# Optimization experiments

Measured on AMD Instinct MI355X. Metric: run time of the kernel, lower is better.

The kernel has to match this reference:

```python
import jax, jax.numpy as jnp
import numpy as np

B, N, D = 32, 4096, 512
H, DH, NS = 8, 64, 16
DI = H * DH
HID = 2048
ITERS = 3
EPS = 1e-8
TAU = 1.0
SCALE = D ** -0.5


def _ln(x, w, b):
    mu = jnp.mean(x, axis=-1, keepdims=True)
    var = jnp.mean(jnp.square(x - mu), axis=-1, keepdims=True)
    return (x - mu) * jax.lax.rsqrt(var + 1e-5) * w + b


def _gumbel_hard(logits, g, tau, axis):
    # straight-through hard gumbel softmax (matches torch F.gumbel_softmax(hard=True))
    y = jax.nn.softmax((logits + g) / tau, axis=axis)
    hard = jax.nn.one_hot(jnp.argmax(y, axis=axis), y.shape[axis], axis=axis, dtype=y.dtype)
    return hard + y - jax.lax.stop_gradient(y)


def setup_inputs():
    key = jax.random.key(0)
    ks = jax.random.split(key, 16)
    w = lambda k, sh: (0.02 * jax.random.normal(k, sh)).astype(jnp.float32)
    gumbel = lambda k, sh: -jnp.log(-jnp.log(jax.random.uniform(k, sh, jnp.float32, 1e-6, 1.0 - 1e-6)))
    return {
        "inputs": jax.random.normal(ks[0], (B, N, D), jnp.float32),
        "slots_mu": jax.random.normal(ks[1], (1, 1, D), jnp.float32),
        "slots_logsigma": (0.05 * jax.random.normal(ks[2], (1, 1, D))).astype(jnp.float32),
        "ln_in_w": jnp.ones((D,), jnp.float32), "ln_in_b": jnp.zeros((D,), jnp.float32),
        "ln_s_w": jnp.ones((D,), jnp.float32), "ln_s_b": jnp.zeros((D,), jnp.float32),
        "ln_ff_w": jnp.ones((D,), jnp.float32), "ln_ff_b": jnp.zeros((D,), jnp.float32),
        "Wq": w(ks[3], (D, DI)), "bq": jnp.zeros((DI,), jnp.float32),
        "Wk": w(ks[4], (D, DI)), "bk": jnp.zeros((DI,), jnp.float32),
        "Wv": w(ks[5], (D, DI)), "bv": jnp.zeros((DI,), jnp.float32),
        "Wc": w(ks[6], (DI, D)), "bc": jnp.zeros((D,), jnp.float32),
        "Wih": w(ks[7], (3 * D, D)), "bih": jnp.zeros((3 * D,), jnp.float32),
        "Whh": w(ks[8], (3 * D, D)), "bhh": jnp.zeros((3 * D,), jnp.float32),
        "W1": w(ks[9], (D, HID)), "b1": jnp.zeros((HID,), jnp.float32),
        "W2": w(ks[10], (HID, D)), "b2": jnp.zeros((D,), jnp.float32),
        "Wkeep": w(ks[11], (D, 2)),
        "slot_noise": jax.random.normal(ks[12], (B, NS, D), jnp.float32),
        "g_keep": gumbel(ks[13], (B, NS, 2)),
        "g_route": gumbel(ks[14], (B, NS, N)),
    }


def reference(inputs, slots_mu, slots_logsigma, ln_in_w, ln_in_b, ln_s_w, ln_s_b,
              ln_ff_w, ln_ff_b, Wq, bq, Wk, bk, Wv, bv, Wc, bc, Wih, bih, Whh, bhh,
              W1, b1, W2, b2, Wkeep, slot_noise, g_keep, g_route):
    b = inputs.shape[0]
    x = _ln(inputs, ln_in_w, ln_in_b)                              # [b,n,d]
    k = (x @ Wk + bk).reshape(b, N, H, DH)                         # [b,n,h,dh]
    v = (x @ Wv + bv).reshape(b, N, H, DH)
    slots = slots_mu + jnp.exp(slots_logsigma) * slot_noise        # [b,ns,d]
    for _ in range(ITERS):
        slots_prev = slots
        s = _ln(slots, ln_s_w, ln_s_b)
        q = (s @ Wq + bq).reshape(b, NS, H, DH)                    # [b,ns,h,dh]
        dots = jnp.einsum('bihd,bjhd->bhij', q, k) * SCALE         # [b,h,ns,n]
        attn = jax.nn.softmax(dots, axis=-2)                       # softmax over slots
        attn = attn + EPS
        attn = attn / jnp.sum(attn, axis=-1, keepdims=True)        # L1-normalize over tokens
        upd = jnp.einsum('bjhd,bhij->bihd', v, attn).reshape(b, NS, DI)
        upd = upd @ Wc + bc                                        # [b,ns,d]
        # PyTorch GRUCell
        gi = upd @ Wih.T + bih
        gh = slots_prev @ Whh.T + bhh
        gi_r, gi_z, gi_n = jnp.split(gi, 3, axis=-1)
        gh_r, gh_z, gh_n = jnp.split(gh, 3, axis=-1)
        r = jax.nn.sigmoid(gi_r + gh_r)
        z = jax.nn.sigmoid(gi_z + gh_z)
        nn_ = jnp.tanh(gi_n + r * gh_n)
        slots = (1.0 - z) * nn_ + z * slots_prev
        h = jax.nn.relu(_ln(slots, ln_ff_w, ln_ff_b) @ W1 + b1)
        slots = slots + h @ W2 + b2
    keep = _gumbel_hard(slots @ Wkeep, g_keep, TAU, axis=-1)[..., -1]  # [b,ns]
    slots = slots * keep[..., None]
    dots2 = jnp.einsum('bid,bjd->bij', slots, x) * SCALE           # [b,ns,n]
    attn2 = _gumbel_hard(dots2, g_route, 1.0, axis=-2)             # hard route over slots
    attn2 = jnp.transpose(attn2, (0, 2, 1))                        # [b,n,ns]
    corr_token = jnp.einsum('bjd,bij->bid', slots, attn2)          # [b,n,d]
    return corr_token
```

## Files before the change

### kernel.cpp

```cpp
#include <hip/hip_runtime.h>
#include <hip/hip_bf16.h>
#include <math.h>

constexpr int Bn = 32, Nn = 4096, Dn = 512, NSn = 16, HIn = 128;
constexpr float kScale = 0.04419417382415922f;
constexpr float kEps = 1e-8f;

typedef __attribute__((ext_vector_type(8))) short short8;
typedef __attribute__((ext_vector_type(4))) float f32x4;

__device__ __forceinline__ float wred(float v) {
#pragma unroll
  for (int m = 32; m > 0; m >>= 1) v += __shfl_xor(v, m);
  return v;
}
__device__ __forceinline__ double wredd(double v) {
#pragma unroll
  for (int m = 32; m > 0; m >>= 1) v += __shfl_xor(v, m);
  return v;
}

__device__ __forceinline__ unsigned short f2bf(float x) {
  unsigned u = __float_as_uint(x);
  unsigned r = (u + 0x7fffu + ((u >> 16) & 1u)) >> 16;
  return (unsigned short)r;
}
__device__ __forceinline__ float bf2f(unsigned short h) {
  return __uint_as_float(((unsigned)h) << 16);
}
__device__ __forceinline__ unsigned packhm(float x) {
  unsigned short h = f2bf(x);
  unsigned short m = f2bf(x - bf2f(h));
  return (unsigned)h | ((unsigned)m << 16);
}
__device__ __forceinline__ unsigned pack2x(float x0, float x1, unsigned& mo) {
  unsigned p0 = packhm(x0), p1 = packhm(x1);
  mo = (p0 >> 16) | (p1 & 0xffff0000u);
  return (p0 & 0xffffu) | (p1 << 16);
}

__global__ __launch_bounds__(256) void k_tsplit(const float* __restrict__ in, unsigned short* __restrict__ inT,
                                                float* __restrict__ psum, float* __restrict__ psqs) {
  __shared__ float tile[64][65];
  int b = blockIdx.z, j0 = blockIdx.x * 64, d0 = blockIdx.y * 64;
  int t = threadIdx.x;
  int rr = t >> 4, c4 = (t & 15) * 4;
  float4 v4[4];
#pragma unroll
  for (int e = 0; e < 4; ++e) {
    int r = e * 16 + rr;
    v4[e] = *reinterpret_cast<const float4*>(&in[((size_t)b * Nn + j0 + r) * Dn + d0 + c4]);
    tile[r][c4] = v4[e].x; tile[r][c4 + 1] = v4[e].y;
    tile[r][c4 + 2] = v4[e].z; tile[r][c4 + 3] = v4[e].w;
  }
  __syncthreads();
  float rs_s, rs_q;
  {
    int r = t >> 2, q = t & 3;
    float s = 0.0f, qq = 0.0f;
#pragma unroll
    for (int c = 0; c < 16; ++c) {
      float x = tile[r][q * 16 + c];
      s += x; qq += x * x;
    }
    s += __shfl_xor(s, 1); s += __shfl_xor(s, 2);
    qq += __shfl_xor(qq, 1); qq += __shfl_xor(qq, 2);
    rs_s = s; rs_q = qq;
  }
  unsigned short pv[16];
#pragma unroll
  for (int e = 0; e < 4; ++e) {
    pv[e * 4 + 0] = f2bf(v4[e].x);
    pv[e * 4 + 1] = f2bf(v4[e].y);
    pv[e * 4 + 2] = f2bf(v4[e].z);
    pv[e * 4 + 3] = f2bf(v4[e].w);
  }
  __syncthreads();
  unsigned short (*u16t)[130] = reinterpret_cast<unsigned short(*)[130]>(tile);
#pragma unroll
  for (int e = 0; e < 4; ++e) {
    int r = e * 16 + rr;
    u16t[r][c4] = pv[e * 4 + 0]; u16t[r][c4 + 1] = pv[e * 4 + 1];
    u16t[r][c4 + 2] = pv[e * 4 + 2]; u16t[r][c4 + 3] = pv[e * 4 + 3];
  }
  {
    int r = t >> 2, q = t & 3;
    if (q == 0) {
      size_t pi = ((size_t)b * Nn + j0 + r) * 8 + blockIdx.y;
      psum[pi] = rs_s;
      psqs[pi] = rs_q;
    }
  }
  __syncthreads();
#pragma unroll
  for (int e = 0; e < 4; ++e) {
    int dloc = e * 16 + rr;
    unsigned short o0 = u16t[c4][dloc], o1 = u16t[c4 + 1][dloc];
    unsigned short o2 = u16t[c4 + 2][dloc], o3 = u16t[c4 + 3][dloc];
    uint2 o;
    o.x = (unsigned)o0 | ((unsigned)o1 << 16);
    o.y = (unsigned)o2 | ((unsigned)o3 << 16);
    *reinterpret_cast<uint2*>(&inT[((size_t)b * Dn + d0 + dloc) * Nn + j0 + c4]) = o;
  }
}

__global__ __launch_bounds__(256) void k_initln(const float* __restrict__ smu, const float* __restrict__ sls,
                                                const float* __restrict__ noise,
                                                const float* __restrict__ lnsw, const float* __restrict__ lnsb,
                                                float* __restrict__ slots, float* __restrict__ sln,
                                                const float* __restrict__ psum, const float* __restrict__ psqs,
                                                float* __restrict__ mu, float* __restrict__ rsig) {
  int t = threadIdx.x;
  if (blockIdx.x >= Bn * NSn) {
    int row = (blockIdx.x - Bn * NSn) * 256 + t;
    float s = 0.0f, q = 0.0f;
#pragma unroll
    for (int e = 0; e < 8; ++e) {
      s += psum[(size_t)row * 8 + e];
      q += psqs[(size_t)row * 8 + e];
    }
    float m = s * (1.0f / 512.0f);
    float var = q * (1.0f / 512.0f) - m * m;
    mu[row] = m;
    rsig[row] = 1.0f / sqrtf(var + 1e-5f);
    return;
  }
  int r = blockIdx.x;
  __shared__ float red[8];
  float sn[2];
#pragma unroll
  for (int j = 0; j < 2; ++j) {
    int c = j * 256 + t;
    sn[j] = smu[c] + expf(sls[c]) * noise[(size_t)r * Dn + c];
  }
  float s = sn[0] + sn[1], q = sn[0] * sn[0] + sn[1] * sn[1];
  s = wred(s); q = wred(q);
  if ((t & 63) == 0) { red[t >> 6] = s; red[4 + (t >> 6)] = q; }
  __syncthreads();
  float S = red[0] + red[1] + red[2] + red[3];
  float Q = red[4] + red[5] + red[6] + red[7];
  float m = S * (1.0f / 512.0f);
  float rs = 1.0f / sqrtf(Q * (1.0f / 512.0f) - m * m + 1e-5f);
#pragma unroll
  for (int j = 0; j < 2; ++j) {
    int c = j * 256 + t;
    slots[(size_t)r * Dn + c] = sn[j];
    sln[(size_t)r * Dn + c] = (sn[j] - m) * rs * lnsw[c] + lnsb[c];
  }
}

template <bool TRANS, bool RELU, bool ADD>
__global__ __launch_bounds__(256) void k_gemm_sm(const float* __restrict__ A, const float* __restrict__ W,
                                                 const float* __restrict__ bias, float* __restrict__ out,
                                                 int Nc, int K) {
  __shared__ float as_[64][17];
  __shared__ float ws_[16][65];
  int m0 = blockIdx.y * 64, n0 = blockIdx.x * 64;
  int t = threadIdx.x, tx = t & 15, ty = t >> 4;
  float acc[4][4] = {};
  float pa[4], pw[4];
  auto loadA = [&](int k0) {
#pragma unroll
    for (int e = 0; e < 4; ++e) {
      int idx = t + e * 256;
      int r = idx >> 4, c = idx & 15;
      pa[e] = A[(size_t)(m0 + r) * K + k0 + c];
    }
  };
  auto loadW = [&](int k0) {
#pragma unroll
    for (int e = 0; e < 4; ++e) {
      int idx = t + e * 256;
      if (!TRANS) {
        int r = idx >> 6, c = idx & 63;
        pw[e] = W[(size_t)(k0 + r) * Nc + n0 + c];
      } else {
        int r = idx >> 4, c = idx & 15;
        pw[e] = W[(size_t)(n0 + r) * K + k0 + c];
      }
    }
  };
  loadA(0); loadW(0);
  for (int k0 = 0; k0 < K; k0 += 16) {
#pragma unroll
    for (int e = 0; e < 4; ++e) {
      int idx = t + e * 256;
      int r = idx >> 4, c = idx & 15;
      as_[r][c] = pa[e];
    }
#pragma unroll
    for (int e = 0; e < 4; ++e) {
      int idx = t + e * 256;
      if (!TRANS) {
        int r = idx >> 6, c = idx & 63;
        ws_[r][c] = pw[e];
      } else {
        int r = idx >> 4, c = idx & 15;
        ws_[c][r] = pw[e];
      }
    }
    __syncthreads();
    if (k0 + 16 < K) { loadA(k0 + 16); loadW(k0 + 16); }
#pragma unroll
    for (int kc = 0; kc < 16; ++kc) {
      float av[4], wv[4];
#pragma unroll
      for (int i = 0; i < 4; ++i) av[i] = as_[ty * 4 + i][kc];
#pragma unroll
      for (int j = 0; j < 4; ++j) wv[j] = ws_[kc][tx * 4 + j];
#pragma unroll
      for (int i = 0; i < 4; ++i)
#pragma unroll
        for (int j = 0; j < 4; ++j) acc[i][j] += av[i] * wv[j];
    }
    __syncthreads();
  }
#pragma unroll
  for (int i = 0; i < 4; ++i)
#pragma unroll
    for (int j = 0; j < 4; ++j) {
      int m = m0 + ty * 4 + i, n = n0 + tx * 4 + j;
      float v = acc[i][j] + (bias ? bias[n] : 0.0f);
      if (RELU) v = fmaxf(v, 0.0f);
      if (ADD) v += out[(size_t)m * Nc + n];
      out[(size_t)m * Nc + n] = v;
    }
}

// ... 315 lines not shown
  }
  float s = sn[0] + sn[1], q = sn[0] * sn[0] + sn[1] * sn[1];
  s = wred(s); q = wred(q);
  if ((t & 63) == 0) { red[t >> 6] = s; red[4 + (t >> 6)] = q; }
  __syncthreads();
  float S = red[0] + red[1] + red[2] + red[3];
  float Q = red[4] + red[5] + red[6] + red[7];
  float m = S * (1.0f / 512.0f);
  float rs = 1.0f / sqrtf(Q * (1.0f / 512.0f) - m * m + 1e-5f);
#pragma unroll
  for (int j = 0; j < 2; ++j) {
    int c = j * 256 + t;
    size_t idx = (size_t)r * 512 + c;
    slots[idx] = sn[j];
    sln[idx] = (sn[j] - m) * rs * lnsw[c] + lnsb[c];
  }
}

__global__ __launch_bounds__(256) void k_mh(const float* __restrict__ Wq, const float* __restrict__ Wk,
                                            float* __restrict__ Ms) {
  int h = blockIdx.z, k0 = blockIdx.y * 64, d0 = blockIdx.x * 64;
  __shared__ float qa[64][65];
  __shared__ float ka[64][65];
  int t = threadIdx.x, tx = t & 15, ty = t >> 4;
#pragma unroll
  for (int e = 0; e < 16; ++e) {
    int idx = t + e * 256;
    int r = idx >> 6, c = idx & 63;
    qa[c][r] = Wq[(size_t)(k0 + r) * Dn + h * 64 + c];
    ka[c][r] = Wk[(size_t)(d0 + r) * Dn + h * 64 + c];
  }
  __syncthreads();
  float acc[4][4] = {};
#pragma unroll 4
  for (int c = 0; c < 64; ++c) {
    float av[4], bv[4];
#pragma unroll
    for (int i = 0; i < 4; ++i) av[i] = qa[c][ty * 4 + i];
#pragma unroll
    for (int j = 0; j < 4; ++j) bv[j] = ka[c][tx * 4 + j];
#pragma unroll
    for (int i = 0; i < 4; ++i)
#pragma unroll
      for (int j = 0; j < 4; ++j) acc[i][j] += av[i] * bv[j];
  }
#pragma unroll
  for (int i = 0; i < 4; ++i)
#pragma unroll
    for (int j = 0; j < 4; ++j)
      Ms[(size_t)(k0 + ty * 4 + i) * 4096 + h * 512 + d0 + tx * 4 + j] = acc[i][j];
}

__global__ __launch_bounds__(256) void k_vbias_bcih(const float* __restrict__ Wk, const float* __restrict__ bq,
                                                    const float* __restrict__ lnw, float* __restrict__ vb_raw,
                                                    float* __restrict__ vb_s, const float* __restrict__ bc,
                                                    const float* __restrict__ Wih, const float* __restrict__ bih,
                                                    float* __restrict__ bcih) {
  __shared__ float cbuf[512];
  int t = threadIdx.x;
  if (blockIdx.x < 2) {
    cbuf[t] = bq[t]; cbuf[256 + t] = bq[256 + t];
    __syncthreads();
    int d = blockIdx.x * 256 + t;
    float vb[8] = {};
    const float4* wr = reinterpret_cast<const float4*>(Wk + (size_t)d * Dn);
#pragma unroll 8
    for (int c4 = 0; c4 < 128; ++c4) {
      float4 wv = wr[c4];
      int h = c4 >> 4;
      int c = c4 * 4;
      vb[h] += wv.x * cbuf[c] + wv.y * cbuf[c + 1] + wv.z * cbuf[c + 2] + wv.w * cbuf[c + 3];
    }
    float lw = lnw[d];
#pragma unroll
    for (int h = 0; h < 8; ++h) {
      vb_raw[h * 512 + d] = vb[h];
      vb_s[h * 512 + d] = kScale * lw * vb[h];
    }
  } else {
    cbuf[t] = bc[t]; cbuf[256 + t] = bc[256 + t];
    __syncthreads();
    int n = (blockIdx.x - 2) * 256 + t;
    const float4* wr = reinterpret_cast<const float4*>(Wih + (size_t)n * Dn);
    float a = 0.0f;
#pragma unroll 8
    for (int c4 = 0; c4 < 128; ++c4) {
      float4 wv = wr[c4];
      int c = c4 * 4;
      a += wv.x * cbuf[c] + wv.y * cbuf[c + 1] + wv.z * cbuf[c + 2] + wv.w * cbuf[c + 3];
    }
    bcih[n] = a + bih[n];
  }
}

__global__ __launch_bounds__(256) void k_mfold_consts(float* __restrict__ Ms, const float* __restrict__ Wq,
                                                      const float* __restrict__ bk, const float* __restrict__ lnw,
                                                      const float* __restrict__ lnb, float* __restrict__ avec,
                                                      float* __restrict__ bvec, const float* __restrict__ vb_raw,
                                                      const float* __restrict__ bq, float* __restrict__ aconst,
                                                      float* __restrict__ bconst) {
  int t = threadIdx.x;
  if (blockIdx.x < 16) {
    __shared__ float lws[512], lbs[512], bks[512];
    lws[t] = lnw[t]; lws[256 + t] = lnw[256 + t];
    lbs[t] = lnb[t]; lbs[256 + t] = lnb[256 + t];
    bks[t] = bk[t]; bks[256 + t] = bk[256 + t];
    __syncthreads();
    int g = blockIdx.x * 256 + t;
    int k = g >> 3, h = g & 7;
    float* mr = Ms + (size_t)k * 4096 + h * 512;
    float mlnb = 0.0f, mlnw = 0.0f;
    for (int d = 0; d < 512; d += 4) {
      float4 m4 = *reinterpret_cast<const float4*>(mr + d);
      mlnb += m4.x * lbs[d] + m4.y * lbs[d + 1] + m4.z * lbs[d + 2] + m4.w * lbs[d + 3];
      mlnw += m4.x * lws[d] + m4.y * lws[d + 1] + m4.z * lws[d + 2] + m4.w * lws[d + 3];
      float4 o4 = {m4.x * kScale * lws[d], m4.y * kScale * lws[d + 1],
                   m4.z * kScale * lws[d + 2], m4.w * kScale * lws[d + 3]};
      *reinterpret_cast<float4*>(mr + d) = o4;
    }
    float wqdot = 0.0f;
    const float* qr = Wq + (size_t)k * Dn + h * 64;
    for (int c = 0; c < 64; c += 4) {
      float4 q4 = *reinterpret_cast<const float4*>(qr + c);
      wqdot += q4.x * bks[h * 64 + c] + q4.y * bks[h * 64 + c + 1] +
               q4.z * bks[h * 64 + c + 2] + q4.w * bks[h * 64 + c + 3];
    }
    avec[h * 512 + k] = kScale * (mlnb + wqdot);
    bvec[h * 512 + k] = kScale * mlnw;
  } else {
    __shared__ float r1[256], r2[256], r3[256];
    for (int h = 0; h < 8; ++h) {
      float p1 = 0.0f, p2 = 0.0f, p3 = 0.0f;
      for (int d = t; d < 512; d += 256) {
        float vr = vb_raw[h * 512 + d];
        p1 += lnb[d] * vr;
        p2 += lnw[d] * vr;
      }
      if (t < 64) p3 = bq[h * 64 + t] * bk[h * 64 + t];
      r1[t] = p1; r2[t] = p2; r3[t] = p3;
      __syncthreads();
      for (int s = 128; s > 0; s >>= 1) {
        if (t < s) { r1[t] += r1[t + s]; r2[t] += r2[t + s]; r3[t] += r3[t + s]; }
        __syncthreads();
      }
      if (t == 0) {
        aconst[h] = kScale * (r1[0] + r3[0]);
        bconst[h] = kScale * r2[0];
      }
      __syncthreads();
    }
  }
}

__global__ __launch_bounds__(256) void k_dots(const unsigned short* __restrict__ inT, const unsigned short* __restrict__ qkt,
                                              const float* __restrict__ alpha, const float* __restrict__ beta,
                                              const float* __restrict__ mu, const float* __restrict__ rsig,
                                              unsigned short* __restrict__ A, float* __restrict__ Spart,
                                              float* __restrict__ c1part) {
  __shared__ __align__(16) unsigned short xs_h[128][40];
  __shared__ __align__(16) unsigned short us_h[128][40];
  __shared__ __align__(16) float redbuf[1536];

  int b = blockIdx.y, jt = blockIdx.x, j0 = jt * 128;
  int t = threadIdx.x, w = t >> 6, l = t & 63;
  int lc = l & 15, lg = l >> 4, koff = lg * 8;
  const size_t tbase = (size_t)b * Dn * Nn + j0;
  const size_t ubase = (size_t)b * HIn * Dn;

  f32x4 acc[2][8];
#pragma unroll
  for (int i = 0; i < 2; ++i)
#pragma unroll
    for (int j2 = 0; j2 < 8; ++j2) acc[i][j2] = {0.0f, 0.0f, 0.0f, 0.0f};

  int xdl = t >> 3;
  int xj4 = (t & 7) * 4;

  uint2 px[4];
  uint2 nu[4];
#pragma unroll
  for (int e = 0; e < 4; ++e)
    px[e] = *reinterpret_cast<const uint2*>(&inT[tbase + (size_t)xdl * Nn + e * 32 + xj4]);
#pragma unroll
  for (int e = 0; e < 4; ++e) {
    int idx = t + e * 256;
    int j = idx >> 3, dg = idx & 7;
    nu[e] = *reinterpret_cast<const uint2*>(&qkt[ubase + (size_t)j * Dn + dg * 4]);
  }

  for (int k0 = 0; k0 < 512; k0 += 32) {
#pragma unroll
    for (int e = 0; e < 4; ++e) {
      const unsigned short* pe = reinterpret_cast<const unsigned short*>(&px[e]);
#pragma unroll
      for (int i = 0; i < 4; ++i) {
        int j = e * 32 + xj4 + i;
        int ds = xdl ^ (((j >> 4) & 3) << 3);
        xs_h[j][ds] = pe[i];
      }
    }
#pragma unroll
    for (int e = 0; e < 4; ++e) {
      int idx = t + e * 256;
      int j = idx >> 3, dg = idx & 7;
      *reinterpret_cast<uint2*>(&us_h[j][dg * 4]) = nu[e];
    }
    if (k0 + 32 < 512) {
#pragma unroll
      for (int e = 0; e < 4; ++e)
        px[e] = *reinterpret_cast<const uint2*>(&inT[tbase + (size_t)(k0 + 32 + xdl) * Nn + e * 32 + xj4]);
#pragma unroll
      for (int e = 0; e < 4; ++e) {
        int idx = t + e * 256;
        int j = idx >> 3, dg = idx & 7;
        nu[e] = *reinterpret_cast<const uint2*>(&qkt[ubase + (size_t)j * Dn + k0 + 32 + dg * 4]);
      }
    }
    __syncthreads();
    int row0 = w * 32 + lc, row1 = row0 + 16;
    int sw0 = ((row0 >> 4) & 3) << 3, sw1 = ((row1 >> 4) & 3) << 3;
    short8 ah0 = *reinterpret_cast<const short8*>(&xs_h[row0][koff ^ sw0]);
    short8 ah1 = *reinterpret_cast<const short8*>(&xs_h[row1][koff ^ sw1]);
#pragma unroll
    for (int ht = 0; ht < 8; ++ht) {
      short8 bh = *reinterpret_cast<const short8*>(&us_h[ht * 16 + lc][koff]);
      acc[0][ht] = __builtin_amdgcn_mfma_f32_16x16x32_bf16(ah0, bh, acc[0][ht], 0, 0, 0);
      acc[1][ht] = __builtin_amdgcn_mfma_f32_16x16x32_bf16(ah1, bh, acc[1][ht], 0, 0, 0);
    }
    __syncthreads();
  }

  float* rsL = redbuf;
  float* muL = rsL + 128;
  float* aL = rsL + 256;
  float* bL = rsL + 384;
  float (*sredS)[128] = reinterpret_cast<float(*)[128]>(rsL + 512);
  float (*sredC)[128] = reinterpret_cast<float(*)[128]>(rsL + 512 + 4 * 128);
  if (t < 128) {
    rsL[t] = rsig[(size_t)b * Nn + j0 + t];
    muL[t] = mu[(size_t)b * Nn + j0 + t];
    aL[t] = alpha[b * HIn + t];
    bL[t] = beta[b * HIn + t];
  }
  __syncthreads();

  float sS[8] = {}, sC[8] = {};
#pragma unroll
  for (int jt2 = 0; jt2 < 2; ++jt2) {
    int jbase = w * 32 + jt2 * 16 + lg * 4;
#pragma unroll
    for (int ht = 0; ht < 8; ++ht) {
      int hi = ht * 16 + lc;
      float av = aL[hi], bv = bL[hi];
      float v[4], rs4[4], mr4[4];
#pragma unroll
      for (int r = 0; r < 4; ++r) {
        int jr = jbase + r;
        rs4[r] = rsL[jr];
        mr4[r] = muL[jr] * rs4[r];
        v[r] = acc[jt2][ht][r] * rs4[r] + av - mr4[r] * bv;
      }
      float mx[4] = {v[0], v[1], v[2], v[3]};
#pragma unroll
      for (int m = 1; m <= 8; m <<= 1)
#pragma unroll
        for (int r = 0; r < 4; ++r) mx[r] = fmaxf(mx[r], __shfl_xor(mx[r], m));
      float e4[4], ss[4];
#pragma unroll
      for (int r = 0; r < 4; ++r) { e4[r] = expf(v[r] - mx[r]); ss[r] = e4[r]; }
#pragma unroll
      for (int m = 1; m <= 8; m <<= 1)
#pragma unroll
        for (int r = 0; r < 4; ++r) ss[r] += __shfl_xor(ss[r], m);
      float ps = 0.0f, pc = 0.0f;
      float p0 = e4[0] / ss[0] + kEps, p1 = e4[1] / ss[1] + kEps;
      float p2 = e4[2] / ss[2] + kEps, p3 = e4[3] / ss[3] + kEps;
      unsigned h01 = (unsigned)f2bf(p0 * rs4[0]) | ((unsigned)f2bf(p1 * rs4[1]) << 16);
      unsigned h23 = (unsigned)f2bf(p2 * rs4[2]) | ((unsigned)f2bf(p3 * rs4[3]) << 16);
      uint2 o2 = {h01, h23};
      ps = p0 + p1 + p2 + p3;
      pc = p0 * mr4[0] + p1 * mr4[1] + p2 * mr4[2] + p3 * mr4[3];
      *reinterpret_cast<uint2*>(&A[(size_t)(b * HIn + hi) * Nn + j0 + jbase]) = o2;
      ps += __shfl_xor(ps, 16); ps += __shfl_xor(ps, 32);
      pc += __shfl_xor(pc, 16); pc += __shfl_xor(pc, 32);
      sS[ht] += ps; sC[ht] += pc;
    }
  }
  if (l < 16) {
#pragma unroll
    for (int ht = 0; ht < 8; ++ht) {
      sredS[w][ht * 16 + l] = sS[ht];
      sredC[w][ht * 16 + l] = sC[ht];
    }
  }
  __syncthreads();
  if (t < 128) {
    float s_ = sredS[0][t] + sredS[1][t] + sredS[2][t] + sredS[3][t];
    float c_ = sredC[0][t] + sredC[1][t] + sredC[2][t] + sredC[3][t];
    int sub = (b * 32 + jt) * HIn + t;
    Spart[sub] = s_;
    c1part[sub] = c_;
  }
}

__global__ __launch_bounds__(256) void k_ax(const unsigned short* __restrict__ Au, const unsigned short* __restrict__ inT,
                                            float* __restrict__ AXp) {
  __shared__ __align__(16) unsigned short as_h[128][40];
  __shared__ __align__(16) unsigned short xs_h[64][40];

  int lid = blockIdx.x + 8 * (blockIdx.y + 2 * blockIdx.z);
  int d0 = (lid >> 6) * 64;
  int rest = lid & 63;
  int kp = rest & 1, b = rest >> 1;

  int t = threadIdx.x, w = t >> 6, l = t & 63;
  int lc = l & 15, lg = l >> 4, koff = lg * 8;
  const size_t abase = (size_t)b * HIn * Nn + (size_t)kp * 2048;
  const size_t xbase = ((size_t)b * Dn + d0) * Nn + (size_t)kp * 2048;

  f32x4 acc[2][4];
#pragma unroll
  for (int i = 0; i < 2; ++i)
#pragma unroll
    for (int j2 = 0; j2 < 4; ++j2) acc[i][j2] = {0.0f, 0.0f, 0.0f, 0.0f};

  uint2 pa[4];
  uint2 px[2];
#pragma unroll
  for (int e = 0; e < 4; ++e) {
    int idx = t + e * 256;
    int hi = idx >> 3, sl = idx & 7;
    pa[e] = *reinterpret_cast<const uint2*>(&Au[abase + (size_t)hi * Nn + sl * 4]);
  }
#pragma unroll
  for (int e = 0; e < 2; ++e) {
    int idx = t + e * 256;
    int d = idx >> 3, jg = idx & 7;
    px[e] = *reinterpret_cast<const uint2*>(&inT[xbase + (size_t)d * Nn + jg * 4]);
  }

  for (int c0 = 0; c0 < 2048; c0 += 32) {
#pragma unroll
    for (int e = 0; e < 4; ++e) {
      int idx = t + e * 256;
      int hi = idx >> 3, sl = idx & 7;
      *reinterpret_cast<uint2*>(&as_h[hi][sl * 4]) = pa[e];
    }
#pragma unroll
    for (int e = 0; e < 2; ++e) {
      int idx = t + e * 256;
      int d = idx >> 3, jg = idx & 7;
      *reinterpret_cast<uint2*>(&xs_h[d][jg * 4]) = px[e];
    }
    if (c0 + 32 < 2048) {
#pragma unroll
      for (int e = 0; e < 4; ++e) {
        int idx = t + e * 256;
        int hi = idx >> 3, sl = idx & 7;
        pa[e] = *reinterpret_cast<const uint2*>(&Au[abase + (size_t)hi * Nn + c0 + 32 + sl * 4]);
      }
#pragma unroll
      for (int e = 0; e < 2; ++e) {
        int idx = t + e * 256;
        int d = idx >> 3, jg = idx & 7;
        px[e] = *reinterpret_cast<const uint2*>(&inT[xbase + (size_t)d * Nn + c0 + 32 + jg * 4]);
      }
    }
    __syncthreads();
    short8 ah0 = *reinterpret_cast<const short8*>(&as_h[w * 32 + lc][koff]);
    short8 ah1 = *reinterpret_cast<const short8*>(&as_h[w * 32 + 16 + lc][koff]);
#pragma unroll
    for (int dt = 0; dt < 4; ++dt) {
      short8 bh = *reinterpret_cast<const short8*>(&xs_h[dt * 16 + lc][koff]);
      acc[0][dt] = __builtin_amdgcn_mfma_f32_16x16x32_bf16(ah0, bh, acc[0][dt], 0, 0, 0);
      acc[1][dt] = __builtin_amdgcn_mfma_f32_16x16x32_bf16(ah1, bh, acc[1][dt], 0, 0, 0);
    }
    __syncthreads();
  }

  const size_t obase = (((size_t)kp * Bn + b) * HIn) * Dn + d0;
#pragma unroll
  for (int jt2 = 0; jt2 < 2; ++jt2) {
#pragma unroll
    for (int dt = 0; dt < 4; ++dt) {
#pragma unroll
      for (int r = 0; r < 4; ++r) {
        int hi = w * 32 + jt2 * 16 + lg * 4 + r;
        int d = dt * 16 + lc;
        AXp[obase + (size_t)hi * Dn + d] = acc[jt2][dt][r];
      }
    }
  }
}

__global__ __launch_bounds__(256) void k_updS(const float* __restrict__ AXp, const float* __restrict__ Spart,
                                              const float* __restrict__ c1part, const float* __restrict__ lnw,
                                              const float* __restrict__ lnb, const float* __restrict__ Wv,
                                              const float* __restrict__ bv, float* __restrict__ upd) {
  int b = blockIdx.y, hi = blockIdx.x, h = hi >> 4, i = hi & 15;
  __shared__ float vx[512];
  __shared__ float red[256];
  __shared__ float sSC[2];
  int t = threadIdx.x;
  if (t < 64) {
    float vs = 0.0f, vc = 0.0f;
    if (t < 32) {
      vs = Spart[(size_t)(b * 32 + t) * HIn + hi];
      vc = c1part[(size_t)(b * 32 + t) * HIn + hi];
    }
    vs = wred(vs); vc = wred(vc);
    if (t == 0) { sSC[0] = vs; sSC[1] = vc; }
  }
  __syncthreads();
  float c1v = sSC[1];
  float invS = 1.0f / sSC[0];
  for (int d = t; d < Dn; d += 256) {
    float G = AXp[((size_t)(0 * Bn + b) * HIn + hi) * Dn + d]
            + AXp[((size_t)(1 * Bn + b) * HIn + hi) * Dn + d];
    vx[d] = lnw[d] * (G - c1v) * invS + lnb[d];
  }
  __syncthreads();
  int cc = t & 63, qd = t >> 6;
  float p = 0.0f;
  for (int d = qd * 128; d < qd * 128 + 128; ++d) p += vx[d] * Wv[(size_t)d * Dn + h * 64 + cc];
  red[t] = p;
  __syncthreads();
  if (qd == 0) {
    float v = red[cc] + red[64 + cc] + red[128 + cc] + red[192 + cc] + bv[h * 64 + cc];
    upd[(size_t)(b * NSn + i) * Dn + h * 64 + cc] = v;
  }
}

__global__ __launch_bounds__(256) void k_gruln(const float* __restrict__ gi, const float* __restrict__ gh,
                                               float* __restrict__ slots, float* __restrict__ slnff,
                                               const float* __restrict__ lnffw, const float* __restrict__ lnffb) {
  int r = blockIdx.x, t = threadIdx.x;
  __shared__ float red[8];
  float sn[2];
#pragma unroll
  for (int j = 0; j < 2; ++j) {
    int c = j * 256 + t;
    float gir = gi[(size_t)r * 1536 + c];
    float giz = gi[(size_t)r * 1536 + 512 + c];
    float gin = gi[(size_t)r * 1536 + 1024 + c];
    float ghr = gh[(size_t)r * 1536 + c];
    float ghz = gh[(size_t)r * 1536 + 512 + c];
    float ghn = gh[(size_t)r * 1536 + 1024 + c];
    float rg = 1.0f / (1.0f + expf(-(gir + ghr)));
    float zg = 1.0f / (1.0f + expf(-(giz + ghz)));
    float ng = tanhf(gin + rg * ghn);
    sn[j] = (1.0f - zg) * ng + zg * slots[(size_t)r * Dn + c];
  }
  float s = sn[0] + sn[1], q = sn[0] * sn[0] + sn[1] * sn[1];
  s = wred(s); q = wred(q);
  if ((t & 63) == 0) { red[t >> 6] = s; red[4 + (t >> 6)] = q; }
  __syncthreads();
  float S = red[0] + red[1] + red[2] + red[3];
  float Q = red[4] + red[5] + red[6] + red[7];
  float m = S * (1.0f / 512.0f);
  float rs = 1.0f / sqrtf(Q * (1.0f / 512.0f) - m * m + 1e-5f);
#pragma unroll
  for (int j = 0; j < 2; ++j) {
    int c = j * 256 + t;
    slots[(size_t)r * Dn + c] = sn[j];
    slnff[(size_t)r * Dn + c] = (sn[j] - m) * rs * lnffw[c] + lnffb[c];
  }
}

__global__ __launch_bounds__(256) void k_route_out(const float* __restrict__ in, const float* __restrict__ slots,
                                                   const float* __restrict__ lnw, const float* __restrict__ lnb,
                                                   const float* __restrict__ Wkeep, const float* __restrict__ gk,
                                                   const float* __restrict__ mu, const float* __restrict__ rsig,
                                                   const float* __restrict__ g_route, float* __restrict__ out) {
  int b = blockIdx.y, j0 = blockIdx.x * 128;
  __shared__ __align__(16) float sl[16 * 516];
  __shared__ __align__(16) float lw[512];
  __shared__ __align__(16) float xs[16][132];
  __shared__ double lgd[128][17];
  __shared__ int besti[128];
  __shared__ double swdL[16], sbdL[16];
  int t = threadIdx.x, tx = t & 15, ty = t >> 4;
  int wv_ = t >> 6, lane = t & 63;

  for (int idx = t; idx < 2048; idx += 256) {
    int i = idx >> 7, c = idx & 127;
    *reinterpret_cast<float4*>(&sl[i * 516 + c * 4]) =
        *reinterpret_cast<const float4*>(&slots[(size_t)(b * NSn + i) * Dn + c * 4]);
  }
  if (t < 128)
    *reinterpret_cast<float4*>(&lw[t * 4]) = *reinterpret_cast<const float4*>(&lnw[t * 4]);
  __syncthreads();

#pragma unroll
  for (int qi = 0; qi < 4; ++qi) {
    int i = wv_ * 4 + qi;
    float* srow = &sl[i * 516];
    float sv[8];
#pragma unroll
    for (int e = 0; e < 8; ++e) sv[e] = srow[lane * 8 + e];
    double d0 = 0.0, d1 = 0.0;
#pragma unroll
    for (int e = 0; e < 8; ++e) {
      int d = lane * 8 + e;
      d0 += (double)sv[e] * (double)Wkeep[d * 2];
      d1 += (double)sv[e] * (double)Wkeep[d * 2 + 1];
    }
    d0 = wredd(d0);
    d1 = wredd(d1);
    int keepi = 0;
    if (lane == 0) keepi = ((d1 + (double)gk[(b * NSn + i) * 2 + 1]) > (d0 + (double)gk[(b * NSn + i) * 2])) ? 1 : 0;
    keepi = __shfl(keepi, 0);
    if (!keepi) {
#pragma unroll
      for (int e = 0; e < 8; ++e) { srow[lane * 8 + e] = 0.0f; sv[e] = 0.0f; }
    }
    double pw = 0.0, pb = 0.0;
#pragma unroll
    for (int e = 0; e < 8; ++e) {
      int d = lane * 8 + e;
      pw += (double)sv[e] * (double)lnw[d];
      pb += (double)sv[e] * (double)lnb[d];
    }
    pw = wredd(pw);
    pb = wredd(pb);
    if (lane == 0) { swdL[i] = pw; sbdL[i] = pb; }
  }

  float acc[8] = {};
  double accd[8] = {};
  const size_t inbase = ((size_t)b * Nn + j0) * Dn;

  float pre[8];
#pragma unroll
  for (int e = 0; e < 8; ++e) {
    int idx = t + e * 256;
    int r = idx >> 4, c = idx & 15;
    pre[e] = in[inbase + (size_t)r * Dn + c];
  }
  __syncthreads();

  for (int k0 = 0; k0 < Dn; k0 += 16) {
#pragma unroll
    for (int e = 0; e < 8; ++e) {
      int idx = t + e * 256;
      int r = idx >> 4, c = idx & 15;
      xs[c][r] = pre[e] * lw[k0 + c];
    }
    __syncthreads();
    float nxt[8] = {};
    if (k0 + 16 < Dn) {
#pragma unroll
      for (int e = 0; e < 8; ++e) {
        int idx = t + e * 256;
        int r = idx >> 4, c = idx & 15;
        nxt[e] = in[inbase + (size_t)r * Dn + k0 + 16 + c];
      }
    }
#pragma unroll
    for (int kc = 0; kc < 16; ++kc) {
      float sv = sl[tx * 516 + k0 + kc];
      float4 x0 = *reinterpret_cast<const float4*>(&xs[kc][ty * 8]);
      float4 x1 = *reinterpret_cast<const float4*>(&xs[kc][ty * 8 + 4]);
      acc[0] += x0.x * sv; acc[1] += x0.y * sv; acc[2] += x0.z * sv; acc[3] += x0.w * sv;
      acc[4] += x1.x * sv; acc[5] += x1.y * sv; acc[6] += x1.z * sv; acc[7] += x1.w * sv;
    }
    if ((k0 & 127) == 112) {
#pragma unroll
      for (int e = 0; e < 8; ++e) { accd[e] += (double)acc[e]; acc[e] = 0.0f; }
    }
#pragma unroll
    for (int e = 0; e < 8; ++e) pre[e] = nxt[e];
    __syncthreads();
  }

  double sw_i = swdL[tx], sb_i = sbdL[tx];
#pragma unroll
  for (int r = 0; r < 8; ++r) {
    int j = ty * 8 + r;
    double rsj = (double)rsig[(size_t)b * Nn + j0 + j];
    double muj = (double)mu[(size_t)b * Nn + j0 + j];
    double g = (double)g_route[((size_t)b * NSn + tx) * Nn + j0 + j];
    lgd[j][tx] = (double)kScale * (rsj * accd[r] + sb_i - muj * rsj * sw_i) + g;
  }
  __syncthreads();
  if (t < 128) {
    double best = lgd[t][0];
    int bi = 0;
#pragma unroll
    for (int i = 1; i < 16; ++i) {
      double v = lgd[t][i];
      if (v > best) { best = v; bi = i; }
    }
    besti[t] = bi;
  }
  __syncthreads();
  for (int idx = t; idx < 128 * 128; idx += 256) {
    int j = idx >> 7, c = idx & 127;
    *reinterpret_cast<float4*>(&out[inbase + (size_t)j * Dn + c * 4]) =
        *reinterpret_cast<const float4*>(&sl[besti[j] * 516 + c * 4]);
  }
}

extern "C" void kernel_launch(void* const* d_in, const int* in_sizes, int n_in,
                              void* d_out, int out_size, void* d_ws, size_t ws_size,
                              hipStream_t stream) {
  (void)in_sizes; (void)n_in; (void)out_size; (void)ws_size;
  const float* in = (const float*)d_in[0];
  const float* slots_mu = (const float*)d_in[1];
  const float* slots_ls = (const float*)d_in[2];
  const float* ln_in_w = (const float*)d_in[3];
  const float* ln_in_b = (const float*)d_in[4];
  const float* ln_s_w = (const float*)d_in[5];
  const float* ln_s_b = (const float*)d_in[6];
  const float* ln_ff_w = (const float*)d_in[7];
  const float* ln_ff_b = (const float*)d_in[8];
  const float* Wq = (const float*)d_in[9];
  const float* bq = (const float*)d_in[10];
  const float* Wk = (const float*)d_in[11];
  const float* bk = (const float*)d_in[12];
  const float* Wv = (const float*)d_in[13];
  const float* bv = (const float*)d_in[14];
  const float* Wc = (const float*)d_in[15];
  const float* bc = (const float*)d_in[16];
  const float* Wih = (const float*)d_in[17];
  const float* bih = (const float*)d_in[18];
  const float* Whh = (const float*)d_in[19];
  const float* bhh = (const float*)d_in[20];
  const float* W1 = (const float*)d_in[21];
  const float* b1 = (const float*)d_in[22];
  const float* W2 = (const float*)d_in[23];
  const float* b2 = (const float*)d_in[24];
  const float* Wkeep = (const float*)d_in[25];
  const float* noise = (const float*)d_in[26];
  const float* g_keep = (const float*)d_in[27];
  const float* g_route = (const float*)d_in[28];
  float* out = (float*)d_out;
  unsigned short* inTu = (unsigned short*)d_out;

  char* wptr = (char*)d_ws;
  auto alloc = [&](size_t bytes) {
    char* p = wptr;
    wptr += (bytes + 255) & ~(size_t)255;
    return p;
  };
  float* mu = (float*)alloc((size_t)Bn * Nn * 4);
  float* rsig = (float*)alloc((size_t)Bn * Nn * 4);
  float* psum = (float*)alloc((size_t)Bn * Nn * 8 * 4);
  float* psqs = (float*)alloc((size_t)Bn * Nn * 8 * 4);
  float* slots = (float*)alloc((size_t)Bn * NSn * Dn * 4);
  float* sln = (float*)alloc((size_t)Bn * NSn * Dn * 4);
  unsigned short* qkt = (unsigned short*)alloc((size_t)Bn * HIn * Dn * 2);
  float* alpha = (float*)alloc((size_t)Bn * HIn * 4);
  float* beta = (float*)alloc((size_t)Bn * HIn * 4);
  unsigned short* Abuf = (unsigned short*)alloc((size_t)Bn * HIn * Nn * 2);
  float* Spart = (float*)alloc((size_t)Bn * 32 * HIn * 4);
  float* c1part = (float*)alloc((size_t)Bn * 32 * HIn * 4);
  float* AXp = (float*)alloc((size_t)2 * Bn * HIn * Dn * 4);
  float* updb = (float*)alloc((size_t)Bn * NSn * Dn * 4);
  float* gibuf = (float*)alloc((size_t)Bn * NSn * 1536 * 4);
  float* ghbuf = (float*)alloc((size_t)Bn * NSn * 1536 * 4);
  float* hbuf = (float*)alloc((size_t)Bn * NSn * 2048 * 4);
  float* ffp = (float*)alloc((size_t)4 * 512 * 512 * 4);
  float* T1 = (float*)alloc((size_t)Dn * 1536 * 4);
  float* WhhT = (float*)alloc((size_t)Dn * 1536 * 4);
  float* bcih = (float*)alloc((size_t)1536 * 4);
  float* Ms = (float*)alloc((size_t)Dn * 4096 * 4);
  float* vb_raw = (float*)alloc((size_t)4096 * 4);
  float* vb_s = (float*)alloc((size_t)4096 * 4);
  float* avec = (float*)alloc((size_t)4096 * 4);
  float* bvec = (float*)alloc((size_t)4096 * 4);
  float* aconst = (float*)alloc((size_t)8 * 4);
  float* bconst = (float*)alloc((size_t)8 * 4);

  k_tsplit<<<dim3(Nn / 64, Dn / 64, Bn), 256, 0, stream>>>(in, inTu, psum, psqs);
  k_gemm_sm<true, false, false><<<dim3(24, 8), 256, 0, stream>>>(Wc, Wih, nullptr, T1, 1536, 512);
  k_transp<<<dim3(512 / 64, 1536 / 64), 256, 0, stream>>>(Whh, WhhT, 1536, 512);
  k_vbias_bcih<<<8, 256, 0, stream>>>(Wk, bq, ln_in_w, vb_raw, vb_s, bc, Wih, bih, bcih);
  k_mh<<<dim3(8, 8, 8), 256, 0, stream>>>(Wq, Wk, Ms);
  k_mfold_consts<<<17, 256, 0, stream>>>(Ms, Wq, bk, ln_in_w, ln_in_b, avec, bvec,
                                         vb_raw, bq, aconst, bconst);
  k_initln<<<Bn * NSn + Bn * Nn / 256, 256, 0, stream>>>(slots_mu, slots_ls, noise, ln_s_w, ln_s_b,
                                                         slots, sln, psum, psqs, mu, rsig);

  for (int it = 0; it < 3; ++it) {
    k_qum_ab<<<dim3(96, 8), 256, 0, stream>>>(sln, Ms, vb_s, qkt, avec, bvec, aconst, bconst, alpha, beta);
    k_dots<<<dim3(Nn / 128, Bn), 256, 0, stream>>>(inTu, qkt, alpha, beta, mu, rsig, Abuf, Spart, c1part);
    k_ax<<<dim3(Dn / 64, 2, Bn), 256, 0, stream>>>(Abuf, inTu, AXp);
    k_updS<<<dim3(HIn, Bn), 256, 0, stream>>>(AXp, Spart, c1part, ln_in_w, ln_in_b, Wv, bv, updb);
    k_ggm<<<dim3(24, 8, 2), 256, 0, stream>>>(updb, T1, bcih, slots, WhhT, bhh, gibuf, ghbuf);
    k_gruln<<<Bn * NSn, 256, 0, stream>>>(gibuf, ghbuf, slots, sln, ln_ff_w, ln_ff_b);
    k_mm<true, false><<<dim3(32, 8, 1), 256, 0, stream>>>(sln, 512, W1, 2048, b1, hbuf, 2048, 512);
    k_mm<false, true><<<dim3(8, 8, 4), 256, 0, stream>>>(hbuf, 2048, W2, 512, nullptr, ffp, 512, 512);
    k_w2ln<<<Bn * NSn, 256, 0, stream>>>(ffp, b2, slots, sln, ln_s_w, ln_s_b);
  }

  k_route_out<<<dim3(Nn / 128, Bn), 256, 0, stream>>>(in, slots, ln_in_w, ln_in_b, Wkeep, g_keep,
                                                      mu, rsig, g_route, out);
}
```

Baseline: 1.071 ms.

## Load MFMA operands directly from global memory, dropping LDS staging in dots and ax

k_tsplit now also writes a row-major bf16 copy of the inputs, so k_dots can read each A-fragment as a contiguous 16-byte global load instead of staging the transposed copy through shared memory. k_ax similarly reads its A and X fragments straight from global memory. Both kernels lose their LDS tiles and per-step barriers. The cost is an extra 128MB bf16 write in the preprocessing kernel, plus global loads that are less coalesced and rely on L2/L1 to serve the operands that several waves share.

```diff
diff --git a/kernel.cpp b/kernel.cpp
--- a/kernel.cpp
+++ b/kernel.cpp
@@ -40,6 +40,7 @@
 }
 
 __global__ __launch_bounds__(256) void k_tsplit(const float* __restrict__ in, unsigned short* __restrict__ inT,
+                                                unsigned short* __restrict__ Xp,
                                                 float* __restrict__ psum, float* __restrict__ psqs) {
   __shared__ float tile[64][65];
   int b = blockIdx.z, j0 = blockIdx.x * 64, d0 = blockIdx.y * 64;
@@ -74,6 +75,14 @@
     pv[e * 4 + 1] = f2bf(v4[e].y);
     pv[e * 4 + 2] = f2bf(v4[e].z);
     pv[e * 4 + 3] = f2bf(v4[e].w);
+  }
+#pragma unroll
+  for (int e = 0; e < 4; ++e) {
+    int r = e * 16 + rr;
+    uint2 o;
+    o.x = (unsigned)pv[e * 4 + 0] | ((unsigned)pv[e * 4 + 1] << 16);
+    o.y = (unsigned)pv[e * 4 + 2] | ((unsigned)pv[e * 4 + 3] << 16);
+    *reinterpret_cast<uint2*>(&Xp[((size_t)b * Nn + j0 + r) * Dn + d0 + c4]) = o;
   }
   __syncthreads();
   unsigned short (*u16t)[130] = reinterpret_cast<unsigned short(*)[130]>(tile);
@@ -695,19 +704,16 @@
   }
 }
 
-__global__ __launch_bounds__(256) void k_dots(const unsigned short* __restrict__ inT, const unsigned short* __restrict__ qkt,
+__global__ __launch_bounds__(256) void k_dots(const unsigned short* __restrict__ Xp, const unsigned short* __restrict__ qkt,
                                               const float* __restrict__ alpha, const float* __restrict__ beta,
                                               const float* __restrict__ mu, const float* __restrict__ rsig,
                                               unsigned short* __restrict__ A, float* __restrict__ Spart,
                                               float* __restrict__ c1part) {
-  __shared__ __align__(16) unsigned short xs_h[128][40];
-  __shared__ __align__(16) unsigned short us_h[128][40];
   __shared__ __align__(16) float redbuf[1536];
 
   int b = blockIdx.y, jt = blockIdx.x, j0 = jt * 128;
   int t = threadIdx.x, w = t >> 6, l = t & 63;
   int lc = l & 15, lg = l >> 4, koff = lg * 8;
-  const size_t tbase = (size_t)b * Dn * Nn + j0;
   const size_t ubase = (size_t)b * HIn * Dn;
 
   f32x4 acc[2][8];
@@ -716,61 +722,21 @@
 #pragma unroll
     for (int j2 = 0; j2 < 8; ++j2) acc[i][j2] = {0.0f, 0.0f, 0.0f, 0.0f};
 
-  int xdl = t >> 3;
-  int xj4 = (t & 7) * 4;
-
-  uint2 px[4];
-  uint2 nu[4];
-#pragma unroll
-  for (int e = 0; e < 4; ++e)
-    px[e] = *reinterpret_cast<const uint2*>(&inT[tbase + (size_t)xdl * Nn + e * 32 + xj4]);
-#pragma unroll
-  for (int e = 0; e < 4; ++e) {
-    int idx = t + e * 256;
-    int j = idx >> 3, dg = idx & 7;
-    nu[e] = *reinterpret_cast<const uint2*>(&qkt[ubase + (size_t)j * Dn + dg * 4]);
-  }
-
+  int row0 = w * 32 + lc, row1 = row0 + 16;
+  const unsigned short* xr0 = &Xp[((size_t)b * Nn + j0 + row0) * Dn + koff];
+  const unsigned short* xr1 = &Xp[((size_t)b * Nn + j0 + row1) * Dn + koff];
+  const unsigned short* ur = &qkt[ubase + (size_t)lc * Dn + koff];
+
+#pragma unroll 4
   for (int k0 = 0; k0 < 512; k0 += 32) {
-#pragma unroll
-    for (int e = 0; e < 4; ++e) {
-      const unsigned short* pe = reinterpret_cast<const unsigned short*>(&px[e]);
-#pragma unroll
-      for (int i = 0; i < 4; ++i) {
-        int j = e * 32 + xj4 + i;
-        int ds = xdl ^ (((j >> 4) & 3) << 3);
-        xs_h[j][ds] = pe[i];
-      }
-    }
-#pragma unroll
-    for (int e = 0; e < 4; ++e) {
-      int idx = t + e * 256;
-      int j = idx >> 3, dg = idx & 7;
-      *reinterpret_cast<uint2*>(&us_h[j][dg * 4]) = nu[e];
-    }
-    if (k0 + 32 < 512) {
-#pragma unroll
-      for (int e = 0; e < 4; ++e)
-        px[e] = *reinterpret_cast<const uint2*>(&inT[tbase + (size_t)(k0 + 32 + xdl) * Nn + e * 32 + xj4]);
-#pragma unroll
-      for (int e = 0; e < 4; ++e) {
-        int idx = t + e * 256;
-        int j = idx >> 3, dg = idx & 7;
-        nu[e] = *reinterpret_cast<const uint2*>(&qkt[ubase + (size_t)j * Dn + k0 + 32 + dg * 4]);
-      }
-    }
-    __syncthreads();
-    int row0 = w * 32 + lc, row1 = row0 + 16;
-    int sw0 = ((row0 >> 4) & 3) << 3, sw1 = ((row1 >> 4) & 3) << 3;
-    short8 ah0 = *reinterpret_cast<const short8*>(&xs_h[row0][koff ^ sw0]);
-    short8 ah1 = *reinterpret_cast<const short8*>(&xs_h[row1][koff ^ sw1]);
+    short8 a0 = *reinterpret_cast<const short8*>(&xr0[k0]);
+    short8 a1 = *reinterpret_cast<const short8*>(&xr1[k0]);
 #pragma unroll
     for (int ht = 0; ht < 8; ++ht) {
-      short8 bh = *reinterpret_cast<const short8*>(&us_h[ht * 16 + lc][koff]);
-      acc[0][ht] = __builtin_amdgcn_mfma_f32_16x16x32_bf16(ah0, bh, acc[0][ht], 0, 0, 0);
-      acc[1][ht] = __builtin_amdgcn_mfma_f32_16x16x32_bf16(ah1, bh, acc[1][ht], 0, 0, 0);
-    }
-    __syncthreads();
+      short8 bh = *reinterpret_cast<const short8*>(&ur[(size_t)(ht * 16) * Dn + k0]);
+      acc[0][ht] = __builtin_amdgcn_mfma_f32_16x16x32_bf16(a0, bh, acc[0][ht], 0, 0, 0);
+      acc[1][ht] = __builtin_amdgcn_mfma_f32_16x16x32_bf16(a1, bh, acc[1][ht], 0, 0, 0);
+    }
   }
 
   float* rsL = redbuf;
@@ -848,9 +814,6 @@
 
 __global__ __launch_bounds__(256) void k_ax(const unsigned short* __restrict__ Au, const unsigned short* __restrict__ inT,
                                             float* __restrict__ AXp) {
-  __shared__ __align__(16) unsigned short as_h[128][40];
-  __shared__ __align__(16) unsigned short xs_h[64][40];
-
   int lid = blockIdx.x + 8 * (blockIdx.y + 2 * blockIdx.z);
   int d0 = (lid >> 6) * 64;
   int rest = lid & 63;
@@ -858,8 +821,6 @@
 
   int t = threadIdx.x, w = t >> 6, l = t & 63;
   int lc = l & 15, lg = l >> 4, koff = lg * 8;
-  const size_t abase = (size_t)b * HIn * Nn + (size_t)kp * 2048;
-  const size_t xbase = ((size_t)b * Dn + d0) * Nn + (size_t)kp * 2048;
 
   f32x4 acc[2][4];
 #pragma unroll
@@ -867,58 +828,21 @@
 #pragma unroll
     for (int j2 = 0; j2 < 4; ++j2) acc[i][j2] = {0.0f, 0.0f, 0.0f, 0.0f};
 
-  uint2 pa[4];
-  uint2 px[2];
-#pragma unroll
-  for (int e = 0; e < 4; ++e) {
-    int idx = t + e * 256;
-    int hi = idx >> 3, sl = idx & 7;
-    pa[e] = *reinterpret_cast<const uint2*>(&Au[abase + (size_t)hi * Nn + sl * 4]);
-  }
-#pragma unroll
-  for (int e = 0; e < 2; ++e) {
-    int idx = t + e * 256;
-    int d = idx >> 3, jg = idx & 7;
-    px[e] = *reinterpret_cast<const uint2*>(&inT[xbase + (size_t)d * Nn + jg * 4]);
-  }
-
+  int hi0 = w * 32 + lc, hi1 = hi0 + 16;
+  const unsigned short* ar0 = &Au[(size_t)b * HIn * Nn + (size_t)hi0 * Nn + (size_t)kp * 2048 + koff];
+  const unsigned short* ar1 = &Au[(size_t)b * HIn * Nn + (size_t)hi1 * Nn + (size_t)kp * 2048 + koff];
+  const unsigned short* xr = &inT[((size_t)b * Dn + d0 + lc) * Nn + (size_t)kp * 2048 + koff];
+
+#pragma unroll 4
   for (int c0 = 0; c0 < 2048; c0 += 32) {
-#pragma unroll
-    for (int e = 0; e < 4; ++e) {
-      int idx = t + e * 256;
-      int hi = idx >> 3, sl = idx & 7;
-      *reinterpret_cast<uint2*>(&as_h[hi][sl * 4]) = pa[e];
-    }
-#pragma unroll
-    for (int e = 0; e < 2; ++e) {
-      int idx = t + e * 256;
-      int d = idx >> 3, jg = idx & 7;
-      *reinterpret_cast<uint2*>(&xs_h[d][jg * 4]) = px[e];
-    }
-    if (c0 + 32 < 2048) {
-#pragma unroll
-      for (int e = 0; e < 4; ++e) {
-        int idx = t + e * 256;
-        int hi = idx >> 3, sl = idx & 7;
-        pa[e] = *reinterpret_cast<const uint2*>(&Au[abase + (size_t)hi * Nn + c0 + 32 + sl * 4]);
-      }
-#pragma unroll
-      for (int e = 0; e < 2; ++e) {
-        int idx = t + e * 256;
-        int d = idx >> 3, jg = idx & 7;
-        px[e] = *reinterpret_cast<const uint2*>(&inT[xbase + (size_t)d * Nn + c0 + 32 + jg * 4]);
-      }
-    }
-    __syncthreads();
-    short8 ah0 = *reinterpret_cast<const short8*>(&as_h[w * 32 + lc][koff]);
-    short8 ah1 = *reinterpret_cast<const short8*>(&as_h[w * 32 + 16 + lc][koff]);
+    short8 a0 = *reinterpret_cast<const short8*>(&ar0[c0]);
+    short8 a1 = *reinterpret_cast<const short8*>(&ar1[c0]);
 #pragma unroll
     for (int dt = 0; dt < 4; ++dt) {
-      short8 bh = *reinterpret_cast<const short8*>(&xs_h[dt * 16 + lc][koff]);
-      acc[0][dt] = __builtin_amdgcn_mfma_f32_16x16x32_bf16(ah0, bh, acc[0][dt], 0, 0, 0);
-      acc[1][dt] = __builtin_amdgcn_mfma_f32_16x16x32_bf16(ah1, bh, acc[1][dt], 0, 0, 0);
-    }
-    __syncthreads();
+      short8 bh = *reinterpret_cast<const short8*>(&xr[(size_t)(dt * 16) * Nn + c0]);
+      acc[0][dt] = __builtin_amdgcn_mfma_f32_16x16x32_bf16(a0, bh, acc[0][dt], 0, 0, 0);
+      acc[1][dt] = __builtin_amdgcn_mfma_f32_16x16x32_bf16(a1, bh, acc[1][dt], 0, 0, 0);
+    }
   }
 
   const size_t obase = (((size_t)kp * Bn + b) * HIn) * Dn + d0;
@@ -1196,6 +1120,7 @@
   float* alpha = (float*)alloc((size_t)Bn * HIn * 4);
   float* beta = (float*)alloc((size_t)Bn * HIn * 4);
   unsigned short* Abuf = (unsigned short*)alloc((size_t)Bn * HIn * Nn * 2);
+  unsigned short* Xp = (unsigned short*)alloc((size_t)Bn * Nn * Dn * 2);
   float* Spart = (float*)alloc((size_t)Bn * 32 * HIn * 4);
   float* c1part = (float*)alloc((size_t)Bn * 32 * HIn * 4);
   float* AXp = (float*)alloc((size_t)2 * Bn * HIn * Dn * 4);
@@ -1215,7 +1140,7 @@
   float* aconst = (float*)alloc((size_t)8 * 4);
   float* bconst = (float*)alloc((size_t)8 * 4);
 
-  k_tsplit<<<dim3(Nn / 64, Dn / 64, Bn), 256, 0, stream>>>(in, inTu, psum, psqs);
+  k_tsplit<<<dim3(Nn / 64, Dn / 64, Bn), 256, 0, stream>>>(in, inTu, Xp, psum, psqs);
   k_gemm_sm<true, false, false><<<dim3(24, 8), 256, 0, stream>>>(Wc, Wih, nullptr, T1, 1536, 512);
   k_transp<<<dim3(512 / 64, 1536 / 64), 256, 0, stream>>>(Whh, WhhT, 1536, 512);
   k_vbias_bcih<<<8, 256, 0, stream>>>(Wk, bq, ln_in_w, vb_raw, vb_s, bc, Wih, bih, bcih);
@@ -1227,7 +1152,7 @@
 
   for (int it = 0; it < 3; ++it) {
     k_qum_ab<<<dim3(96, 8), 256, 0, stream>>>(sln, Ms, vb_s, qkt, avec, bvec, aconst, bconst, alpha, beta);
-    k_dots<<<dim3(Nn / 128, Bn), 256, 0, stream>>>(inTu, qkt, alpha, beta, mu, rsig, Abuf, Spart, c1part);
+    k_dots<<<dim3(Nn / 128, Bn), 256, 0, stream>>>(Xp, qkt, alpha, beta, mu, rsig, Abuf, Spart, c1part);
     k_ax<<<dim3(Dn / 64, 2, Bn), 256, 0, stream>>>(Abuf, inTu, AXp);
     k_updS<<<dim3(HIn, Bn), 256, 0, stream>>>(AXp, Spart, c1part, ln_in_w, ln_in_b, Wv, bv, updb);
     k_ggm<<<dim3(24, 8, 2), 256, 0, stream>>>(updb, T1, bcih, slots, WhhT, bhh, gibuf, ghbuf);
```

After: 1.565 ms. 1.46x slower.
